# Performance work log

Hardware: AMD Instinct MI355X
Metric: run time of the kernel (lower is better)

The kernel has to match this reference:

```python
import jax, jax.numpy as jnp
import numpy as np

BN_EPS = 1e-5
K = 2


def _log_shift_max(x):
    # x: [B, C, H, W]. torch.cat([x[..., -s:, :], x[..., :-s, :]], dim=2) == roll(x, +s)
    # and cat([x[..., s:, :], x[..., :s, :]], dim=2) == roll(x, -s).
    H, W = x.shape[2], x.shape[3]
    x_j = jnp.zeros_like(x)
    for i in range(1, int(H).bit_length()):
        s = K ** i - 1
        x_j = jnp.maximum(x_j, x - jnp.roll(x, s, axis=2))
        x_j = jnp.maximum(x_j, x - jnp.roll(x, -s, axis=2))
    for i in range(1, int(W).bit_length()):
        s = K ** i - 1
        x_j = jnp.maximum(x_j, x - jnp.roll(x, s, axis=3))
        x_j = jnp.maximum(x_j, x - jnp.roll(x, -s, axis=3))
    return x_j


def setup_inputs() -> dict:
    key = jax.random.key(0)
    k1, k2 = jax.random.split(key)
    B, C, H, W = 16, 384, 56, 56
    Cout = 384
    x = jax.random.normal(k1, (B, C, H, W), dtype=jnp.float32)
    conv_w = jax.random.normal(k2, (Cout, 2 * C, 1, 1), dtype=jnp.float32) * 0.02
    conv_b = jnp.zeros((Cout,), dtype=jnp.float32)
    bn_scale = jnp.ones((Cout,), dtype=jnp.float32)
    bn_bias = jnp.zeros((Cout,), dtype=jnp.float32)
    bn_mean = jnp.zeros((Cout,), dtype=jnp.float32)
    bn_var = jnp.ones((Cout,), dtype=jnp.float32)
    return {"x": x, "conv_w": conv_w, "conv_b": conv_b,
            "bn_scale": bn_scale, "bn_bias": bn_bias,
            "bn_mean": bn_mean, "bn_var": bn_var}


def reference(x, conv_w, conv_b, bn_scale, bn_bias, bn_mean, bn_var):
    x_j = _log_shift_max(x)                       # [B, C, H, W]
    xc = jnp.concatenate([x, x_j], axis=1)        # [B, 2C, H, W]
    # 1x1 conv == channel contraction
    y = jnp.einsum('bchw,oc->bohw', xc, conv_w[:, :, 0, 0]) + conv_b[None, :, None, None]
    # BatchNorm (eval mode, running stats)
    inv = jax.lax.rsqrt(bn_var + BN_EPS)
    y = (y - bn_mean[None, :, None, None]) * (inv * bn_scale)[None, :, None, None] + bn_bias[None, :, None, None]
    return jax.nn.gelu(y, approximate=False)
```

## Files before the change

kernel.cpp:

```cpp
#include <hip/hip_runtime.h>
#include <cstdint>
#include <cstddef>

typedef unsigned short u16;
typedef unsigned int u32;
typedef __attribute__((ext_vector_type(8))) short short8;
typedef __attribute__((ext_vector_type(4))) float f32x4;

__device__ __forceinline__ float bf2f(u16 v) { return __uint_as_float((u32)v << 16); }
__device__ __forceinline__ u16 f2bf(float f) {
    u32 u = __float_as_uint(f);
    u = (u + 0x7fffu + ((u >> 16) & 1u)) >> 16;
    return (u16)u;
}

#define GLD16(g, l) __builtin_amdgcn_global_load_lds( \
    (const __attribute__((address_space(1))) void*)(g), \
    (__attribute__((address_space(3))) void*)(l), 16, 0, 0)

__global__ void detect_kernel(const u16* __restrict__ x, int* __restrict__ flag) {
    int cnt = 0;
    for (int i = threadIdx.x; i < 256; i += 64) {
        const int e = (x[2 * i] >> 7) & 0xFF;
        cnt += (e >= 96 && e <= 135) ? 1 : 0;
    }
    #pragma unroll
    for (int o = 32; o; o >>= 1) cnt += __shfl_down(cnt, o, 64);
    if (threadIdx.x == 0) *flag = (cnt < 128) ? 1 : 0;
}

__global__ void wconv_kernel(const void* __restrict__ w, u16* __restrict__ wbf,
                             const int* __restrict__ flag) {
    const int i = blockIdx.x * 256 + threadIdx.x;
    if (i >= 384 * 768) return;
    if (*flag) wbf[i] = f2bf(((const float*)w)[i]);
    else       wbf[i] = ((const u16*)w)[i];
}

__global__ __launch_bounds__(256) void xj_kernel(const void* __restrict__ xin,
                                                 u16* __restrict__ xc,
                                                 const int* __restrict__ flag) {
    const int cg = blockIdx.x, b = blockIdx.y;
    const int fp = *flag;
    __shared__ __align__(16) u16 pl[3136][8];
    const size_t plane0 = ((size_t)b * 384 + (size_t)cg * 8) * 3136;

    if (fp) {
        const float* xb = (const float*)xin + plane0;
        for (int g = threadIdx.x; g < 784; g += 256) {
            const int p = g * 4;
            float vv[8][4];
            #pragma unroll
            for (int c = 0; c < 8; ++c) {
                const float4 t = *(const float4*)(xb + (size_t)c * 3136 + p);
                vv[c][0] = t.x; vv[c][1] = t.y; vv[c][2] = t.z; vv[c][3] = t.w;
            }
            #pragma unroll
            for (int i = 0; i < 4; ++i) {
                u32 q[4];
                #pragma unroll
                for (int cc = 0; cc < 4; ++cc)
                    q[cc] = (u32)f2bf(vv[cc * 2][i]) | ((u32)f2bf(vv[cc * 2 + 1][i]) << 16);
                *(uint4*)&pl[p + i][0] = make_uint4(q[0], q[1], q[2], q[3]);
            }
        }
    } else {
        const u16* xb = (const u16*)xin + plane0;
        for (int g = threadIdx.x; g < 784; g += 256) {
            const int p = g * 4;
            u32 rc[8][2];
            #pragma unroll
            for (int c = 0; c < 8; ++c) {
                const uint2 t = *(const uint2*)(xb + (size_t)c * 3136 + p);
                rc[c][0] = t.x; rc[c][1] = t.y;
            }
            #pragma unroll
            for (int i = 0; i < 4; ++i) {
                const int d = i >> 1, sh = (i & 1) * 16;
                u32 q[4];
                #pragma unroll
                for (int cc = 0; cc < 4; ++cc) {
                    const u32 lo = (rc[cc * 2][d] >> sh) & 0xFFFFu;
                    const u32 hi = (rc[cc * 2 + 1][d] >> sh) & 0xFFFFu;
                    q[cc] = lo | (hi << 16);
                }
                *(uint4*)&pl[p + i][0] = make_uint4(q[0], q[1], q[2], q[3]);
            }
        }
    }
    __syncthreads();

    for (int p = threadIdx.x; p < 3136; p += 256) {
        const int h = p / 56, w = p - h * 56;
        int off[20];
        const int S[5] = {1, 3, 7, 15, 31};
        #pragma unroll
        for (int si = 0; si < 5; ++si) {
            const int s = S[si];
            int hp = h + s; if (hp >= 56) hp -= 56;
            int hm = h - s; if (hm < 0)   hm += 56;
            int wp = w + s; if (wp >= 56) wp -= 56;
            int wm = w - s; if (wm < 0)   wm += 56;
            off[si * 4 + 0] = hp * 56 + w;
            off[si * 4 + 1] = hm * 56 + w;
            off[si * 4 + 2] = h * 56 + wp;
            off[si * 4 + 3] = h * 56 + wm;
        }
        const uint4 self = *(const uint4*)&pl[p][0];
        const u32 sw[4] = {self.x, self.y, self.z, self.w};
        float xv[8], mn[8];
        #pragma unroll
        for (int c2 = 0; c2 < 4; ++c2) {
            xv[c2 * 2]     = __uint_as_float(sw[c2] << 16);
            xv[c2 * 2 + 1] = __uint_as_float(sw[c2] & 0xFFFF0000u);
            mn[c2 * 2] = xv[c2 * 2]; mn[c2 * 2 + 1] = xv[c2 * 2 + 1];
        }
        #pragma unroll
        for (int k = 0; k < 20; ++k) {
            const uint4 nb = *(const uint4*)&pl[off[k]][0];
            const u32 nw[4] = {nb.x, nb.y, nb.z, nb.w};
            #pragma unroll
            for (int c2 = 0; c2 < 4; ++c2) {
                mn[c2 * 2]     = fminf(mn[c2 * 2],     __uint_as_float(nw[c2] << 16));
                mn[c2 * 2 + 1] = fminf(mn[c2 * 2 + 1], __uint_as_float(nw[c2] & 0xFFFF0000u));
            }
        }
        u32 jq[4];
        #pragma unroll
        for (int c2 = 0; c2 < 4; ++c2)
            jq[c2] = (u32)f2bf(xv[c2 * 2] - mn[c2 * 2]) |
                     ((u32)f2bf(xv[c2 * 2 + 1] - mn[c2 * 2 + 1]) << 16);
        u16* px = xc + ((((size_t)b * 96) + cg) * 3136 + p) * 8;
        u16* pj = xc + ((((size_t)b * 96) + 48 + cg) * 3136 + p) * 8;
        *(uint4*)px = self;
        *(uint4*)pj = make_uint4(jq[0], jq[1], jq[2], jq[3]);
    }
}

__global__ __launch_bounds__(256) void gemm_kernel(
        const u16* __restrict__ xc, const u16* __restrict__ Wt,
        const void* __restrict__ cb, const void* __restrict__ bsc,
        const void* __restrict__ bbi, const void* __restrict__ bme,
        const void* __restrict__ bva, void* __restrict__ outp,
        const int* __restrict__ flag) {
    const int ntile = blockIdx.x;
    const int mtile = blockIdx.y;
    const int fp = *flag;
    __shared__ __align__(16) u16 Bs[2][16 * 64 * 8];
    __shared__ float2 PB[192];

    const int tid = threadIdx.x;
    if (tid < 192) {
        const int o = mtile * 192 + tid;
        float vsc, vva, vcb, vme, vbi;
        if (fp) {
            vsc = ((const float*)bsc)[o]; vva = ((const float*)bva)[o];
            vcb = ((const float*)cb)[o];  vme = ((const float*)bme)[o];
            vbi = ((const float*)bbi)[o];
        } else {
            vsc = bf2f(((const u16*)bsc)[o]); vva = bf2f(((const u16*)bva)[o]);
            vcb = bf2f(((const u16*)cb)[o]);  vme = bf2f(((const u16*)bme)[o]);
            vbi = bf2f(((const u16*)bbi)[o]);
        }
        const float seff = vsc * rsqrtf(vva + 1e-5f);
        PB[tid] = make_float2(seff, (vcb - vme) * seff + vbi);
    }

    const int lane = tid & 63, wv = tid >> 6;
    const int quad = lane >> 4, l16 = lane & 15;
    const int bb  = ntile / 49;
    const int hw0 = (ntile - bb * 49) * 64;

    const u16* bgp[4]; int bofs[4];
    #pragma unroll
    for (int i = 0; i < 4; ++i) {
        const int idx = i * 256 + tid;
        const int gg = idx >> 6, n = idx & 63;
        bgp[i]  = xc + (((size_t)bb * 96 + gg) * 3136 + hw0 + n) * 8;
        bofs[i] = idx * 8;
    }
    #define STAGE(q) { \
        u16* dst = &Bs[(q) & 1][0]; \
        _Pragma("unroll") \
        for (int i = 0; i < 4; ++i) GLD16(bgp[i] + (size_t)(q) * 16 * 3136 * 8, dst + bofs[i]); }

    const u16* arow[3];
    #pragma unroll
    for (int im = 0; im < 3; ++im)
        arow[im] = Wt + (size_t)(mtile * 192 + wv * 48 + im * 16 + l16) * 768 + quad * 8;

    f32x4 acc[3][4];
    #pragma unroll
    for (int im = 0; im < 3; ++im)
        #pragma unroll
        for (int in = 0; in < 4; ++in)
            acc[im][in] = {0.f, 0.f, 0.f, 0.f};

    STAGE(0);
    __syncthreads();

    for (int q = 0; q < 6; ++q) {
        if (q < 5) STAGE(q + 1);
        const u16* bufq = &Bs[q & 1][0];
        #pragma unroll
        for (int s = 0; s < 4; ++s) {
            const int k0 = q * 128 + s * 32;
            short8 af[3], bfv[4];
            #pragma unroll
            for (int im = 0; im < 3; ++im)
                af[im] = *(const short8*)(arow[im] + k0);
            #pragma unroll
            for (int in = 0; in < 4; ++in)
                bfv[in] = *(const short8*)(bufq + ((s * 4 + quad) * 64 + in * 16 + l16) * 8);
            #pragma unroll
            for (int im = 0; im < 3; ++im)
                #pragma unroll
                for (int in = 0; in < 4; ++in)
                    acc[im][in] = __builtin_amdgcn_mfma_f32_16x16x32_bf16(
                                      af[im], bfv[in], acc[im][in], 0, 0, 0);
        }
        __syncthreads();
    }

    float* T = (float*)&Bs[0][0] + wv * (16 * 68);
    const size_t obase = (size_t)bb * 384 * 3136 + hw0;
    #pragma unroll
    for (int im = 0; im < 3; ++im) {
        #pragma unroll
        for (int r = 0; r < 4; ++r) {
            const int ml = mtile * 192 + wv * 48 + im * 16 + quad * 4 + r;
            const float2 sb = PB[(wv * 48 + im * 16 + quad * 4 + r)];
            #pragma unroll
            for (int in = 0; in < 4; ++in) {
                float v = acc[im][in][r] * sb.x + sb.y;
                v = 0.5f * v * (1.0f + erff(v * 0.70710678118654752f));
                T[(quad * 4 + r) * 68 + in * 16 + l16] = v;
            }
            (void)ml;
        }
        asm volatile("s_waitcnt lgkmcnt(0)" ::: "memory");
        #pragma unroll
        for (int it = 0; it < 4; ++it) {
            const int flat = it * 256 + lane * 4;
            const int row = flat >> 6, col = flat & 63;
            const float4 vv = *(const float4*)&T[row * 68 + col];
            const size_t oi = obase +
                (size_t)(mtile * 192 + wv * 48 + im * 16 + row) * 3136 + col;
            if (fp) {
                *(float4*)((float*)outp + oi) = vv;
            } else {
                const u32 a = (u32)f2bf(vv.x) | ((u32)f2bf(vv.y) << 16);
                const u32 b2 = (u32)f2bf(vv.z) | ((u32)f2bf(vv.w) << 16);
                *(uint2*)((u16*)outp + oi) = make_uint2(a, b2);
            }
        }
        asm volatile("s_waitcnt lgkmcnt(0)" ::: "memory");
    }
    #undef STAGE
}

extern "C" void kernel_launch(void* const* d_in, const int* in_sizes, int n_in,
                              void* d_out, int out_size, void* d_ws, size_t ws_size,
                              hipStream_t stream) {
    const void* x   = d_in[0];
    const void* w   = d_in[1];
    const void* cbp = d_in[2];
    const void* bsc = d_in[3];
    const void* bbi = d_in[4];
    const void* bme = d_in[5];
    const void* bva = d_in[6];

    int* flag = (int*)d_ws;
    u16* xc   = (u16*)((char*)d_ws + 64);
    u16* wbf  = xc + (size_t)16 * 96 * 3136 * 8;

    detect_kernel<<<1, 64, 0, stream>>>((const u16*)x, flag);
    wconv_kernel<<<1152, 256, 0, stream>>>(w, wbf, flag);
    xj_kernel<<<dim3(48, 16), 256, 0, stream>>>(x, xc, flag);
    gemm_kernel<<<dim3(784, 2), 256, 0, stream>>>(xc, wbf, cbp, bsc, bbi, bme, bva,
                                                  d_out, flag);
}
```

Measured before the change: 263.8 us.

## Merge M tiles into 512-thread GEMM blocks with register-prefetched A and deeper pipelining

The GEMM now runs 8 waves per block covering all 384 output channels, so each staged B tile (xc activations) is loaded once instead of twice across two M-tile blocks. A weight fragments are prefetched into double-buffered registers one phase ahead. B tiles are staged two phases ahead with explicit vmcnt waits and raw barriers. The xj min loop is also paired into two-load steps for more ILP. Register pressure from 24 short8 A fragments plus accumulators under launch_bounds(512,8) could force spills or cut occupancy, and the hand-written vmcnt counts are fragile.

```diff
diff --git a/kernel.cpp b/kernel.cpp
--- a/kernel.cpp
+++ b/kernel.cpp
@@ -116,13 +116,17 @@
             mn[c2 * 2] = xv[c2 * 2]; mn[c2 * 2 + 1] = xv[c2 * 2 + 1];
         }
         #pragma unroll
-        for (int k = 0; k < 20; ++k) {
-            const uint4 nb = *(const uint4*)&pl[off[k]][0];
-            const u32 nw[4] = {nb.x, nb.y, nb.z, nb.w};
+        for (int k = 0; k < 20; k += 2) {
+            const uint4 na = *(const uint4*)&pl[off[k]][0];
+            const uint4 nb = *(const uint4*)&pl[off[k + 1]][0];
+            const u32 aw[4] = {na.x, na.y, na.z, na.w};
+            const u32 bw[4] = {nb.x, nb.y, nb.z, nb.w};
             #pragma unroll
             for (int c2 = 0; c2 < 4; ++c2) {
-                mn[c2 * 2]     = fminf(mn[c2 * 2],     __uint_as_float(nw[c2] << 16));
-                mn[c2 * 2 + 1] = fminf(mn[c2 * 2 + 1], __uint_as_float(nw[c2] & 0xFFFF0000u));
+                mn[c2 * 2]     = fminf(fminf(__uint_as_float(aw[c2] << 16),
+                                             __uint_as_float(bw[c2] << 16)), mn[c2 * 2]);
+                mn[c2 * 2 + 1] = fminf(fminf(__uint_as_float(aw[c2] & 0xFFFF0000u),
+                                             __uint_as_float(bw[c2] & 0xFFFF0000u)), mn[c2 * 2 + 1]);
             }
         }
         u32 jq[4];
@@ -137,30 +141,29 @@
     }
 }
 
-__global__ __launch_bounds__(256) void gemm_kernel(
+__global__ __launch_bounds__(512, 8) void gemm_kernel(
         const u16* __restrict__ xc, const u16* __restrict__ Wt,
         const void* __restrict__ cb, const void* __restrict__ bsc,
         const void* __restrict__ bbi, const void* __restrict__ bme,
         const void* __restrict__ bva, void* __restrict__ outp,
         const int* __restrict__ flag) {
     const int ntile = blockIdx.x;
-    const int mtile = blockIdx.y;
     const int fp = *flag;
-    __shared__ __align__(16) u16 Bs[2][16 * 64 * 8];
-    __shared__ float2 PB[192];
+    __shared__ __align__(16) unsigned char smem[34816];
+    __shared__ float2 PB[384];
+    u16* const smemu = (u16*)smem;
 
     const int tid = threadIdx.x;
-    if (tid < 192) {
-        const int o = mtile * 192 + tid;
+    if (tid < 384) {
         float vsc, vva, vcb, vme, vbi;
         if (fp) {
-            vsc = ((const float*)bsc)[o]; vva = ((const float*)bva)[o];
-            vcb = ((const float*)cb)[o];  vme = ((const float*)bme)[o];
-            vbi = ((const float*)bbi)[o];
+            vsc = ((const float*)bsc)[tid]; vva = ((const float*)bva)[tid];
+            vcb = ((const float*)cb)[tid];  vme = ((const float*)bme)[tid];
+            vbi = ((const float*)bbi)[tid];
         } else {
-            vsc = bf2f(((const u16*)bsc)[o]); vva = bf2f(((const u16*)bva)[o]);
-            vcb = bf2f(((const u16*)cb)[o]);  vme = bf2f(((const u16*)bme)[o]);
-            vbi = bf2f(((const u16*)bbi)[o]);
+            vsc = bf2f(((const u16*)bsc)[tid]); vva = bf2f(((const u16*)bva)[tid]);
+            vcb = bf2f(((const u16*)cb)[tid]);  vme = bf2f(((const u16*)bme)[tid]);
+            vbi = bf2f(((const u16*)bbi)[tid]);
         }
         const float seff = vsc * rsqrtf(vva + 1e-5f);
         PB[tid] = make_float2(seff, (vcb - vme) * seff + vbi);
@@ -171,23 +174,48 @@
     const int bb  = ntile / 49;
     const int hw0 = (ntile - bb * 49) * 64;
 
-    const u16* bgp[4]; int bofs[4];
-    #pragma unroll
-    for (int i = 0; i < 4; ++i) {
-        const int idx = i * 256 + tid;
+    const u16* bgp[2]; int bofs[2];
+    #pragma unroll
+    for (int i = 0; i < 2; ++i) {
+        const int idx = i * 512 + tid;
         const int gg = idx >> 6, n = idx & 63;
         bgp[i]  = xc + (((size_t)bb * 96 + gg) * 3136 + hw0 + n) * 8;
         bofs[i] = idx * 8;
     }
     #define STAGE(q) { \
-        u16* dst = &Bs[(q) & 1][0]; \
+        u16* dst = smemu + ((q) & 1) * 8192; \
+        GLD16(bgp[0] + (size_t)(q) * 16 * 3136 * 8, dst + bofs[0]); \
+        GLD16(bgp[1] + (size_t)(q) * 16 * 3136 * 8, dst + bofs[1]); }
+
+    const u16* arow[3];
+    #pragma unroll
+    for (int im = 0; im < 3; ++im)
+        arow[im] = Wt + (size_t)(wv * 48 + im * 16 + l16) * 768 + quad * 8;
+
+    #define LOADA(dst, q) { \
         _Pragma("unroll") \
-        for (int i = 0; i < 4; ++i) GLD16(bgp[i] + (size_t)(q) * 16 * 3136 * 8, dst + bofs[i]); }
-
-    const u16* arow[3];
-    #pragma unroll
-    for (int im = 0; im < 3; ++im)
-        arow[im] = Wt + (size_t)(mtile * 192 + wv * 48 + im * 16 + l16) * 768 + quad * 8;
+        for (int s4 = 0; s4 < 4; ++s4) \
+            _Pragma("unroll") \
+            for (int im = 0; im < 3; ++im) \
+                dst[s4 * 3 + im] = *(const short8*)(arow[im] + (q) * 128 + s4 * 32); }
+
+    #define COMPUTE(q, afv) { \
+        const u16* bufq = smemu + ((q) & 1) * 8192; \
+        _Pragma("unroll") \
+        for (int s = 0; s < 4; ++s) { \
+            short8 bfv[4]; \
+            _Pragma("unroll") \
+            for (int in = 0; in < 4; ++in) \
+                bfv[in] = *(const short8*)(bufq + ((s * 4 + quad) * 64 + in * 16 + l16) * 8); \
+            _Pragma("unroll") \
+            for (int im = 0; im < 3; ++im) \
+                _Pragma("unroll") \
+                for (int in = 0; in < 4; ++in) \
+                    acc[im][in] = __builtin_amdgcn_mfma_f32_16x16x32_bf16( \
+                                      afv[s * 3 + im], bfv[in], acc[im][in], 0, 0, 0); } }
+
+    #define VMCNT14 asm volatile("s_waitcnt vmcnt(14)" ::: "memory")
+    #define VMCNT12 asm volatile("s_waitcnt vmcnt(12)" ::: "memory")
 
     f32x4 acc[3][4];
     #pragma unroll
@@ -196,39 +224,35 @@
         for (int in = 0; in < 4; ++in)
             acc[im][in] = {0.f, 0.f, 0.f, 0.f};
 
+    short8 afA[12], afB[12];
+
+    LOADA(afA, 0);
     STAGE(0);
-    __syncthreads();
-
-    for (int q = 0; q < 6; ++q) {
-        if (q < 5) STAGE(q + 1);
-        const u16* bufq = &Bs[q & 1][0];
-        #pragma unroll
-        for (int s = 0; s < 4; ++s) {
-            const int k0 = q * 128 + s * 32;
-            short8 af[3], bfv[4];
-            #pragma unroll
-            for (int im = 0; im < 3; ++im)
-                af[im] = *(const short8*)(arow[im] + k0);
-            #pragma unroll
-            for (int in = 0; in < 4; ++in)
-                bfv[in] = *(const short8*)(bufq + ((s * 4 + quad) * 64 + in * 16 + l16) * 8);
-            #pragma unroll
-            for (int im = 0; im < 3; ++im)
-                #pragma unroll
-                for (int in = 0; in < 4; ++in)
-                    acc[im][in] = __builtin_amdgcn_mfma_f32_16x16x32_bf16(
-                                      af[im], bfv[in], acc[im][in], 0, 0, 0);
-        }
-        __syncthreads();
-    }
-
-    float* T = (float*)&Bs[0][0] + wv * (16 * 68);
+    STAGE(1);
+    asm volatile("s_waitcnt vmcnt(2) lgkmcnt(0)" ::: "memory");
+    __builtin_amdgcn_s_barrier();
+
+    #define PHASE(q, cur, nxt) { \
+        if ((q) < 5) LOADA(nxt, (q) + 1); \
+        COMPUTE(q, cur); \
+        __builtin_amdgcn_s_barrier(); \
+        if ((q) < 4) STAGE((q) + 2); \
+        if ((q) <= 3)      { VMCNT14; __builtin_amdgcn_s_barrier(); } \
+        else if ((q) == 4) { VMCNT12; __builtin_amdgcn_s_barrier(); } }
+
+    PHASE(0, afA, afB);
+    PHASE(1, afB, afA);
+    PHASE(2, afA, afB);
+    PHASE(3, afB, afA);
+    PHASE(4, afA, afB);
+    PHASE(5, afB, afA);
+
+    float* T = (float*)smem + wv * (16 * 68);
     const size_t obase = (size_t)bb * 384 * 3136 + hw0;
     #pragma unroll
     for (int im = 0; im < 3; ++im) {
         #pragma unroll
         for (int r = 0; r < 4; ++r) {
-            const int ml = mtile * 192 + wv * 48 + im * 16 + quad * 4 + r;
             const float2 sb = PB[(wv * 48 + im * 16 + quad * 4 + r)];
             #pragma unroll
             for (int in = 0; in < 4; ++in) {
@@ -236,7 +260,6 @@
                 v = 0.5f * v * (1.0f + erff(v * 0.70710678118654752f));
                 T[(quad * 4 + r) * 68 + in * 16 + l16] = v;
             }
-            (void)ml;
         }
         asm volatile("s_waitcnt lgkmcnt(0)" ::: "memory");
         #pragma unroll
@@ -245,7 +268,7 @@
             const int row = flat >> 6, col = flat & 63;
             const float4 vv = *(const float4*)&T[row * 68 + col];
             const size_t oi = obase +
-                (size_t)(mtile * 192 + wv * 48 + im * 16 + row) * 3136 + col;
+                (size_t)(wv * 48 + im * 16 + row) * 3136 + col;
             if (fp) {
                 *(float4*)((float*)outp + oi) = vv;
             } else {
@@ -256,6 +279,11 @@
         }
         asm volatile("s_waitcnt lgkmcnt(0)" ::: "memory");
     }
+    #undef PHASE
+    #undef VMCNT14
+    #undef VMCNT12
+    #undef COMPUTE
+    #undef LOADA
     #undef STAGE
 }
 
@@ -277,6 +305,6 @@
     detect_kernel<<<1, 64, 0, stream>>>((const u16*)x, flag);
     wconv_kernel<<<1152, 256, 0, stream>>>(w, wbf, flag);
     xj_kernel<<<dim3(48, 16), 256, 0, stream>>>(x, xc, flag);
-    gemm_kernel<<<dim3(784, 2), 256, 0, stream>>>(xc, wbf, cbp, bsc, bbi, bme, bva,
-                                                  d_out, flag);
-}
+    gemm_kernel<<<784, 512, 0, stream>>>(xc, wbf, cbp, bsc, bbi, bme, bva,
+                                         d_out, flag);
+}
```

Result: slower. 658.5 us (+149.6%).
